# Kernel optimization log

Measured on AMD Instinct MI355X. Metric: run time of the kernel, lower is better.

Reference implementation:

```python
import jax, jax.numpy as jnp
import numpy as np

B, DIM, HH, WW = 8, 512, 64, 64
HEADS, DH = 8, 64
INNER = HEADS * DH
EPS = 1e-5  # ChanLayerNorm2D eps


def _chan_norm(x, g, b):
    # channel-wise layernorm over axis 1 (biased variance, like torch.var(unbiased=False))
    m = jnp.mean(x, axis=1, keepdims=True)
    v = jnp.mean((x - m) ** 2, axis=1, keepdims=True)
    return (x - m) / jnp.sqrt(v + EPS) * g + b


def _l2norm(x):
    # F.normalize(dim=1), eps=1e-12
    n = jnp.sqrt(jnp.sum(x * x, axis=1, keepdims=True))
    return x / jnp.maximum(n, 1e-12)


def setup_inputs() -> dict:
    key = jax.random.key(0)
    ks = jax.random.split(key, 10)
    sc = 1.0 / np.sqrt(DIM)
    return {
        "context": jax.random.normal(ks[0], (B, DIM, HH, WW), jnp.float32),
        "query_source": jax.random.normal(ks[1], (B, DIM, HH, WW), jnp.float32),
        "ctx_g": jnp.ones((1, DIM, 1, 1), jnp.float32),
        "ctx_b": jnp.zeros((1, DIM, 1, 1), jnp.float32),
        "qs_g": jnp.ones((1, DIM, 1, 1), jnp.float32),
        "qs_b": jnp.zeros((1, DIM, 1, 1), jnp.float32),
        "w_q": jax.random.normal(ks[2], (INNER, DIM), jnp.float32) * sc,
        "w_kv": jax.random.normal(ks[3], (2 * INNER, DIM), jnp.float32) * sc,
        "w_out": jax.random.normal(ks[4], (DIM, INNER), jnp.float32) * (1.0 / np.sqrt(INNER)),
        "gamma": jax.random.normal(ks[5], (1,), jnp.float32) * 0.5,
    }


def reference(context, query_source, ctx_g, ctx_b, qs_g, qs_b, w_q, w_kv, w_out, gamma):
    b, c, height, width = query_source.shape
    kh = int(height ** 0.5)  # default height_top_k
    kw = int(width ** 0.5)   # default width_top_k

    ctx = _chan_norm(context, ctx_g, ctx_b)
    qs = _chan_norm(query_source, qs_g, qs_b)

    # 1x1 convs as GEMMs
    kv = jnp.einsum('oi,bihw->bohw', w_kv, ctx)
    k, v = jnp.split(kv, 2, axis=1)
    q = jnp.einsum('oi,bihw->bohw', w_q, qs)

    def fold(t):  # b (h c) H W -> (b h) c H W
        return t.reshape(b, HEADS, DH, height, width).reshape(b * HEADS, DH, height, width)

    q, k, v = fold(q), fold(k), fold(v)
    q, k = _l2norm(q), _l2norm(k)

    # dual pruning (kh < height and kw < width here)
    q_abs = jnp.abs(q)
    k_abs = jnp.abs(k)
    q_probe = jnp.sum(q_abs, axis=(2, 3))            # (bh, c)

    # height selection
    k_height = jnp.sum(k_abs, axis=3)                # (bh, c, H)
    score_r = jnp.einsum('bc,bch->bh', q_probe, k_height)
    _, idx_h = jax.lax.top_k(score_r, kh)            # (bh, kh)
    k = jnp.take_along_axis(k, idx_h[:, None, :, None], axis=2)
    v = jnp.take_along_axis(v, idx_h[:, None, :, None], axis=2)

    # width selection (scores use pre-height-gather k_abs, as in original)
    k_width = jnp.sum(k_abs, axis=2)                 # (bh, c, W)
    score_c = jnp.einsum('bc,bcw->bw', q_probe, k_width)
    _, idx_w = jax.lax.top_k(score_c, kw)            # (bh, kw)
    k = jnp.take_along_axis(k, idx_w[:, None, None, :], axis=3)
    v = jnp.take_along_axis(v, idx_w[:, None, None, :], axis=3)

    def flat(t):  # (bh) d h w -> (bh) (h w) d
        bh, d, h_, w_ = t.shape
        return t.transpose(0, 2, 3, 1).reshape(bh, h_ * w_, d)

    qf, kf, vf = flat(q), flat(k), flat(v)
    attn = jax.nn.softmax(jnp.einsum('bid,bjd->bij', qf, kf), axis=-1)
    out = jnp.einsum('bij,bjd->bid', attn, vf)       # (bh, H*W, d)

    out = out.reshape(b, HEADS, height, width, DH).transpose(0, 1, 4, 2, 3)
    out = out.reshape(b, INNER, height, width)
    out = jnp.einsum('oi,bihw->bohw', w_out, out)
    return gamma[0] * out + qs
```

## Files before the change

### kernel.cpp

```cpp
#include <hip/hip_runtime.h>
#include <math.h>

#define HW 4096
#define DIM 512

typedef __attribute__((ext_vector_type(8))) short short8;
typedef __attribute__((ext_vector_type(4))) float f32x4;

__device__ inline unsigned short f2bf(float f) {
    unsigned int u = __float_as_uint(f);
    u += 0x7fff + ((u >> 16) & 1);
    return (unsigned short)(u >> 16);
}
__device__ inline float bf2f(unsigned short h) {
    return __uint_as_float(((unsigned int)h) << 16);
}
__device__ inline unsigned pack2(float a, float b) {
    return (unsigned)f2bf(a) | ((unsigned)f2bf(b) << 16);
}

__device__ inline void gld16(const void* g, void* lds) {
    __builtin_amdgcn_global_load_lds(
        (const __attribute__((address_space(1))) unsigned int*)g,
        (__attribute__((address_space(3))) unsigned int*)lds, 16, 0, 0);
}

__global__ void prep_weights(const float* __restrict__ w_q, const float* __restrict__ w_kv,
                             const float* __restrict__ w_out,
                             const float* __restrict__ ctx_g, const float* __restrict__ ctx_b,
                             const float* __restrict__ qs_g, const float* __restrict__ qs_b,
                             unsigned short* __restrict__ wq_b, unsigned short* __restrict__ wk_b,
                             unsigned short* __restrict__ wo_b, float* __restrict__ wv_g,
                             float* __restrict__ Avec, float* __restrict__ Cvec)
{
    int blk = blockIdx.x;
    int widx = blk >> 9;
    int o = blk & 511;
    int tid = threadIdx.x;
    const float *src, *g = nullptr, *beta = nullptr;
    if (widx == 0)      { src = w_q  + (size_t)o * DIM; g = qs_g;  beta = qs_b; }
    else if (widx == 1) { src = w_kv + (size_t)o * DIM; g = ctx_g; beta = ctx_b; }
    else if (widx == 2) { src = w_kv + (size_t)(512 + o) * DIM; g = ctx_g; beta = ctx_b; }
    else                { src = w_out + (size_t)o * DIM; }
    float a = 0.f, c = 0.f;
    for (int i = tid; i < DIM; i += 256) {
        float w = src[i];
        if (widx == 3) { wo_b[(size_t)o * DIM + i] = f2bf(w); continue; }
        float wg = w * g[i];
        if (widx == 0)      wq_b[(size_t)o * DIM + i] = f2bf(wg);
        else if (widx == 1) wk_b[(size_t)o * DIM + i] = f2bf(wg);
        else                wv_g[(size_t)o * DIM + i] = wg;
        a += wg; c += w * beta[i];
    }
    if (widx == 3) return;
    __shared__ float sa[256], sc[256];
    sa[tid] = a; sc[tid] = c;
    __syncthreads();
    for (int s = 128; s > 0; s >>= 1) {
        if (tid < s) { sa[tid] += sa[tid + s]; sc[tid] += sc[tid + s]; }
        __syncthreads();
    }
    if (tid == 0) { Avec[widx * 512 + o] = sa[0]; Cvec[widx * 512 + o] = sc[0]; }
}

__global__ __launch_bounds__(256) void conv_stats(
    const float* __restrict__ ctx, const float* __restrict__ qs,
    unsigned short* __restrict__ ctx_t, unsigned short* __restrict__ qs_t,
    float* __restrict__ ctx_m, float* __restrict__ ctx_r,
    float* __restrict__ qs_m, float* __restrict__ qs_r)
{
    int which = blockIdx.z;
    int b = blockIdx.y;
    int p0 = blockIdx.x * 32;
    const float* X = (which ? qs : ctx) + (size_t)b * DIM * HW;
    unsigned short* Xt = (which ? qs_t : ctx_t) + (size_t)b * HW * DIM;
    int tid = threadIdx.x;
    int pg = tid & 7;
    int cR = tid >> 3;

    const float* src0 = X + p0 + pg * 4;

    float4 s4 = {0.f, 0.f, 0.f, 0.f};
    float4 q4 = {0.f, 0.f, 0.f, 0.f};
    float4 buf[2][8];

#pragma unroll
    for (int it = 0; it < 2; it++)
#pragma unroll
        for (int j = 0; j < 8; j++)
            buf[it][j] = *(const float4*)(src0 + (size_t)(it * 256 + cR * 8 + j) * HW);

#pragma unroll
    for (int it = 0; it < 2; it++) {
        unsigned short* dst = Xt + (size_t)(p0 + pg * 4) * 512 + it * 256 + cR * 8;
        uint4 o;
        o.x = pack2(buf[it][0].x, buf[it][1].x);
        o.y = pack2(buf[it][2].x, buf[it][3].x);
        o.z = pack2(buf[it][4].x, buf[it][5].x);
        o.w = pack2(buf[it][6].x, buf[it][7].x);
        *(uint4*)(dst) = o;
        o.x = pack2(buf[it][0].y, buf[it][1].y);
        o.y = pack2(buf[it][2].y, buf[it][3].y);
        o.z = pack2(buf[it][4].y, buf[it][5].y);
        o.w = pack2(buf[it][6].y, buf[it][7].y);
        *(uint4*)(dst + 512) = o;
        o.x = pack2(buf[it][0].z, buf[it][1].z);
        o.y = pack2(buf[it][2].z, buf[it][3].z);
        o.z = pack2(buf[it][4].z, buf[it][5].z);
        o.w = pack2(buf[it][6].z, buf[it][7].z);
        *(uint4*)(dst + 1024) = o;
        o.x = pack2(buf[it][0].w, buf[it][1].w);
        o.y = pack2(buf[it][2].w, buf[it][3].w);
        o.z = pack2(buf[it][4].w, buf[it][5].w);
        o.w = pack2(buf[it][6].w, buf[it][7].w);
        *(uint4*)(dst + 1536) = o;
#pragma unroll
        for (int j = 0; j < 8; j++) {
            float4 v = buf[it][j];
            s4.x += v.x; s4.y += v.y; s4.z += v.z; s4.w += v.w;
            q4.x = fmaf(v.x, v.x, q4.x);
            q4.y = fmaf(v.y, v.y, q4.y);
            q4.z = fmaf(v.z, v.z, q4.z);
            q4.w = fmaf(v.w, v.w, q4.w);
        }
    }

#pragma unroll
    for (int off = 8; off <= 32; off <<= 1) {
        s4.x += __shfl_xor(s4.x, off, 64);
        s4.y += __shfl_xor(s4.y, off, 64);
        s4.z += __shfl_xor(s4.z, off, 64);
        s4.w += __shfl_xor(s4.w, off, 64);
        q4.x += __shfl_xor(q4.x, off, 64);
        q4.y += __shfl_xor(q4.y, off, 64);
        q4.z += __shfl_xor(q4.z, off, 64);
        q4.w += __shfl_xor(q4.w, off, 64);
    }

    __shared__ float sRed[4 * 32], qRed[4 * 32];
    int wave = tid >> 6, lane = tid & 63;
    if (lane < 8) {
        int base = wave * 32 + lane * 4;
        sRed[base + 0] = s4.x; sRed[base + 1] = s4.y;
        sRed[base + 2] = s4.z; sRed[base + 3] = s4.w;
        qRed[base + 0] = q4.x; qRed[base + 1] = q4.y;
        qRed[base + 2] = q4.z; qRed[base + 3] = q4.w;
    }
    __syncthreads();
    if (tid < 32) {
        float s = sRed[tid] + sRed[32 + tid] + sRed[64 + tid] + sRed[96 + tid];
        float q = qRed[tid] + qRed[32 + tid] + qRed[64 + tid] + qRed[96 + tid];
        float m = s * (1.0f / DIM);
        float var = q * (1.0f / DIM) - m * m;
        float r = 1.0f / sqrtf(var + 1e-5f);
        int pix = b * HW + p0 + tid;
        if (which == 0) { ctx_m[pix] = m; ctx_r[pix] = r; }
        else            { qs_m[pix]  = m; qs_r[pix]  = r; }
    }
}

template<int MODE>
__global__ __launch_bounds__(256) void gemm_mfma(
    const unsigned short* __restrict__ Wb, const unsigned short* __restrict__ Xt,
    float* __restrict__ Y, unsigned short* __restrict__ Ybf,
    const float* __restrict__ mean, const float* __restrict__ rstd,
    const float* __restrict__ Arow, const float* __restrict__ Crow,
    float* __restrict__ probe,
    const float* __restrict__ qsrc, const float* __restrict__ g,
    const float* __restrict__ beta, const float* __restrict__ gammaPtr)
{
    int b = blockIdx.z;
    int n0 = blockIdx.x * 128;
    int m0 = blockIdx.y * 128;
    const unsigned short* Xb = Xt + (size_t)b * HW * DIM;
    __shared__ uint4 AsBuf[512];
    __shared__ uint4 BsBuf[512];
    unsigned short* As = (unsigned short*)AsBuf;
    unsigned short* Bs = (unsigned short*)BsBuf;
    int tid = threadIdx.x;
    int lane = tid & 63;
    int wave = tid >> 6;
    int wbase = tid & 192;
    int wm = (wave >> 1) * 64;
    int wn = (wave & 1) * 64;
    int quad = lane >> 4;
    int l16 = lane & 15;

    int r0 = tid >> 2, c0 = (tid & 3) * 8;
    const unsigned short* pA0 = Wb + (size_t)(m0 + r0) * DIM + c0;
    const unsigned short* pA1 = Wb + (size_t)(m0 + 64 + r0) * DIM + c0;
    const unsigned short* pB0 = Xb + (size_t)(n0 + r0) * DIM + c0;
    const unsigned short* pB1 = Xb + (size_t)(n0 + 64 + r0) * DIM + c0;

    f32x4 acc[4][4];
#pragma unroll
    for (int i = 0; i < 4; i++)
#pragma unroll
        for (int j = 0; j < 4; j++) acc[i][j] = (f32x4){0.f, 0.f, 0.f, 0.f};

    for (int kt = 0; kt < 16; kt++) {
        gld16(pA0, AsBuf + wbase);
        gld16(pA1, AsBuf + 256 + wbase);
        gld16(pB0, BsBuf + wbase);
        gld16(pB1, BsBuf + 256 + wbase);
        pA0 += 32; pA1 += 32; pB0 += 32; pB1 += 32;
        __syncthreads();
        short8 af[4], bfr[4];
#pragma unroll
        for (int i = 0; i < 4; i++)
            af[i] = *(const short8*)(As + (wm + i * 16 + l16) * 32 + quad * 8);
#pragma unroll
        for (int j = 0; j < 4; j++)
            bfr[j] = *(const short8*)(Bs + (wn + j * 16 + l16) * 32 + quad * 8);
#pragma unroll
        for (int i = 0; i < 4; i++)
#pragma unroll
            for (int j = 0; j < 4; j++)
                acc[i][j] = __builtin_amdgcn_mfma_f32_16x16x32_bf16(af[i], bfr[j], acc[i][j], 0, 0, 0);
        __syncthreads();
    }

    if (MODE < 2) {
        float pa[4][4] = {};
#pragma unroll
        for (int j = 0; j < 4; j++) {
            int n = n0 + wn + j * 16 + l16;
            int pix = b * HW + n;
            float mn = mean[pix], rs = rstd[pix];
            float y[4][4];
            float s2 = 0.f;
#pragma unroll
            for (int i = 0; i < 4; i++) {
                int mb = m0 + wm + i * 16 + quad * 4;
#pragma unroll
                for (int r = 0; r < 4; r++) {
                    float v = rs * (acc[i][j][r] - mn * Arow[mb + r]) + Crow[mb + r];
                    y[i][r] = v;
                    s2 = fmaf(v, v, s2);
                }
            }
            s2 += __shfl_xor(s2, 16, 64);
            s2 += __shfl_xor(s2, 32, 64);
            float inv = 1.0f / fmaxf(sqrtf(s2), 1e-12f);
            unsigned short* orow = Ybf + (size_t)(b * HW + n) * 512 + m0 + wm + quad * 4;
#pragma unroll
            for (int i = 0; i < 4; i++) {
                float v0 = y[i][0] * inv, v1 = y[i][1] * inv;
                float v2 = y[i][2] * inv, v3 = y[i][3] * inv;
                uint2 pk; pk.x = pack2(v0, v1); pk.y = pack2(v2, v3);
                *(uint2*)(orow + i * 16) = pk;
                pa[i][0] += fabsf(v0); pa[i][1] += fabsf(v1);
                pa[i][2] += fabsf(v2); pa[i][3] += fabsf(v3);
            }
        }
#pragma unroll
        for (int i = 0; i < 4; i++)
#pragma unroll
            for (int r = 0; r < 4; r++) {
                float v = pa[i][r];
                v += __shfl_xor(v, 1, 64);
                v += __shfl_xor(v, 2, 64);
                v += __shfl_xor(v, 4, 64);
                v += __shfl_xor(v, 8, 64);
                pa[i][r] = v;
            }
        if (l16 == 0) {
#pragma unroll
            for (int i = 0; i < 4; i++)
#pragma unroll
                for (int r = 0; r < 4; r++) {
                    int m = m0 + wm + i * 16 + quad * 4 + r;
                    if (MODE == 0) atomicAdd(&probe[b * 512 + m], pa[i][r]);
                    else atomicAdd(&probe[(size_t)(b * 512 + m) * 64 + ((n0 + wn) >> 6)], pa[i][r]);
                }
        }
    } else {
        float* Yb = Y + (size_t)b * DIM * HW;
        float gamma = gammaPtr[0];
        const float* qb = qsrc + (size_t)b * DIM * HW;
#pragma unroll
        for (int j = 0; j < 4; j++) {
            int n = n0 + wn + j * 16 + l16;
            int pix = b * HW + n;
            float mn = mean[pix], rs = rstd[pix];
#pragma unroll
            for (int i = 0; i < 4; i++) {
                int mb = m0 + wm + i * 16 + quad * 4;
#pragma unroll
                for (int r = 0; r < 4; r++) {
                    int m = mb + r;
                    float qn = (qb[(size_t)m * HW + n] - mn) * rs * g[m] + beta[m];
                    Yb[(size_t)m * HW + n] = gamma * acc[i][j][r] + qn;
                }
            }
        }
    }
}

__global__ __launch_bounds__(256) void kws_kernel(const unsigned short* __restrict__ kbf,
                                                  float* __restrict__ kws)
{
    int blk = blockIdx.x;
    int b = blk >> 6, w = blk & 63;
    int tid = threadIdx.x;
    int c8 = tid & 63;
    int hq = tid >> 6;
    float a[8] = {};
    for (int hh = 0; hh < 16; hh++) {
        const unsigned short* row = kbf + ((size_t)(b * HW + (hq * 16 + hh) * 64 + w)) * 512 + c8 * 8;
        uint4 pk = *(const uint4*)row;
        const unsigned short* u = (const unsigned short*)&pk;
#pragma unroll
        for (int j = 0; j < 8; j++) a[j] += fabsf(bf2f(u[j]));
    }
    __shared__ float red[512 * 4];
#pragma unroll
    for (int j = 0; j < 8; j++) red[(c8 * 8 + j) * 4 + hq] = a[j];
    __syncthreads();
    if (tid < 256) {
        int c = tid;
        float v0 = red[c * 4] + red[c * 4 + 1] + red[c * 4 + 2] + red[c * 4 + 3];
        int c2 = tid + 256;
        float v1 = red[c2 * 4] + red[c2 * 4 + 1] + red[c2 * 4 + 2] + red[c2 * 4 + 3];
        kws[(size_t)(b * 512 + c) * 64 + w] = v0;
        kws[(size_t)(b * 512 + c2) * 64 + w] = v1;
    }
}

__global__ void score_topk(const float* __restrict__ qp, const float* __restrict__ khs,
                           const float* __restrict__ kws, int* __restrict__ idx_h, int* __restrict__ idx_w)
{
    int bh = blockIdx.x;
    int lane = threadIdx.x;
    float sr = 0.f, sc = 0.f;
    for (int c = 0; c < 64; c++) {
        float q = qp[bh * 64 + c];
        sr = fmaf(q, khs[(size_t)(bh * 64 + c) * 64 + lane], sr);
        sc = fmaf(q, kws[(size_t)(bh * 64 + c) * 64 + lane], sc);
    }
    float v = sr;
    for (int it = 0; it < 8; it++) {
        float bv = v; int bi = lane;
        for (int off = 1; off < 64; off <<= 1) {
            float ov = __shfl_xor(bv, off, 64);
            int oi = __shfl_xor(bi, off, 64);
            if (ov > bv || (ov == bv && oi < bi)) { bv = ov; bi = oi; }
        }
        if (lane == 0) idx_h[bh * 8 + it] = bi;
        if (lane == bi) v = -INFINITY;
    }
    v = sc;
    for (int it = 0; it < 8; it++) {
        float bv = v; int bi = lane;
        for (int off = 1; off < 64; off <<= 1) {
            float ov = __shfl_xor(bv, off, 64);
            int oi = __shfl_xor(bi, off, 64);
            if (ov > bv || (ov == bv && oi < bi)) { bv = ov; bi = oi; }
        }
        if (lane == 0) idx_w[bh * 8 + it] = bi;
        if (lane == bi) v = -INFINITY;
    }
}

__global__ void gather_kv(const unsigned short* __restrict__ kbf, const unsigned short* __restrict__ ctx_t,
                          const float* __restrict__ wv_g, const float* __restrict__ Av, const float* __restrict__ Cv,
                          const float* __restrict__ ctx_m, const float* __restrict__ ctx_r,
                          const int* __restrict__ idx_h, const int* __restrict__ idx_w,
                          unsigned short* __restrict__ kg, unsigned short* __restrict__ vgt)
{
    int blk = blockIdx.x;
    int bh = blk >> 6, j = blk & 63;
    int h = idx_h[bh * 8 + (j >> 3)];
    int w = idx_w[bh * 8 + (j & 7)];
    int p = h * 64 + w;
    int b = bh >> 3, head = bh & 7;
    int d = threadIdx.x;
    kg[(size_t)blk * 64 + d] = kbf[(size_t)(b * HW + p) * 512 + head * 64 + d];
    __shared__ float cx[DIM];
    const unsigned short* crow = ctx_t + (size_t)(b * HW + p) * 512;
    short8 cv = ((const short8*)crow)[d];
#pragma unroll
    for (int u = 0; u < 8; u++) cx[d * 8 + u] = bf2f((unsigned short)cv[u]);
    __syncthreads();
    int o = head * 64 + d;
    const float* wrow = wv_g + (size_t)o * DIM;
    float acc = 0.f;
    for (int i = 0; i < DIM; i++) acc = fmaf(wrow[i], cx[i], acc);
    int pix = b * HW + p;
    float v = ctx_r[pix] * (acc - ctx_m[pix] * Av[o]) + Cv[o];
    vgt[((size_t)bh * 64 + d) * 64 + j] = f2bf(v);
}

#define PROW 72
__global__ __launch_bounds__(256) void attn_mfma(
    const unsigned short* __restrict__ qbf, const unsigned short* __restrict__ kg,
    const unsigned short* __restrict__ vgt, unsigned short* __restrict__ abuf)
{
    int bh = blockIdx.y;
    int b = bh >> 3, head = bh & 7;
    int tid = threadIdx.x;
    int lane = tid & 63, wave = tid >> 6;
    int g = lane >> 4, l16 = lane & 15;
    int p0 = blockIdx.x * 256 + wave * 64;

    __shared__ unsigned short Plds[4][64 * PROW];
    unsigned short* P = Plds[wave];

    const unsigned short* kgb = kg + (size_t)bh * 4096;
    const unsigned short* vtb = vgt + (size_t)bh * 4096;
    const unsigned short* qb = qbf + (size_t)(b * HW) * 512 + head * 64;

    short8 Qf[4][2];
#pragma unroll
    for (int j = 0; j < 4; j++)
#pragma unroll
        for (int t = 0; t < 2; t++)
            Qf[j][t] = *(const short8*)(qb + (size_t)(p0 + j * 16 + l16) * 512 + t * 32 + g * 8);

    f32x4 S[4][4];
#pragma unroll
    for (int i = 0; i < 4; i++)
#pragma unroll
        for (int j = 0; j < 4; j++) S[i][j] = (f32x4){0.f, 0.f, 0.f, 0.f};
#pragma unroll
    for (int t = 0; t < 2; t++) {
        short8 Kf[4];
#pragma unroll
        for (int i = 0; i < 4; i++)
            Kf[i] = *(const short8*)(kgb + (i * 16 + l16) * 64 + t * 32 + g * 8);
#pragma unroll
        for (int i = 0; i < 4; i++)
#pragma unroll
            for (int j = 0; j < 4; j++)
                S[i][j] = __builtin_amdgcn_mfma_f32_16x16x32_bf16(Kf[i], Qf[j][t], S[i][j], 0, 0, 0);
    }

    float inv[4];
#pragma unroll
    for (int j = 0; j < 4; j++) {
        float e[4][4];
        float s = 0.f;
#pragma unroll
        for (int i = 0; i < 4; i++)
#pragma unroll
            for (int r = 0; r < 4; r++) { e[i][r] = __expf(S[i][j][r]); s += e[i][r]; }
        s += __shfl_xor(s, 16, 64);
        s += __shfl_xor(s, 32, 64);
        inv[j] = 1.0f / s;
        int row = j * 16 + l16;
#pragma unroll
        for (int i = 0; i < 4; i++) {
            uint2 pk;
            pk.x = pack2(e[i][0], e[i][1]);
            pk.y = pack2(e[i][2], e[i][3]);
            *(uint2*)(P + row * PROW + i * 16 + g * 4) = pk;
        }
    }

    f32x4 O[4][4];
#pragma unroll
    for (int i = 0; i < 4; i++)
#pragma unroll
        for (int j = 0; j < 4; j++) O[i][j] = (f32x4){0.f, 0.f, 0.f, 0.f};
#pragma unroll
    for (int t = 0; t < 2; t++) {
        short8 Vf[4], Pf[4];
#pragma unroll
        for (int i = 0; i < 4; i++)
            Vf[i] = *(const short8*)(vtb + (i * 16 + l16) * 64 + t * 32 + g * 8);
#pragma unroll
        for (int j = 0; j < 4; j++)
            Pf[j] = *(const short8*)(P + (j * 16 + l16) * PROW + t * 32 + g * 8);
#pragma unroll
        for (int i = 0; i < 4; i++)
#pragma unroll
            for (int j = 0; j < 4; j++)
                O[i][j] = __builtin_amdgcn_mfma_f32_16x16x32_bf16(Vf[i], Pf[j], O[i][j], 0, 0, 0);
    }

    unsigned short* ob = abuf + (size_t)(b * HW) * 512 + head * 64;
#pragma unroll
    for (int j = 0; j < 4; j++) {
        int p = p0 + j * 16 + l16;
#pragma unroll
        for (int i = 0; i < 4; i++) {
            uint2 pk;
            pk.x = pack2(O[i][j][0] * inv[j], O[i][j][1] * inv[j]);
            pk.y = pack2(O[i][j][2] * inv[j], O[i][j][3] * inv[j]);
            *(uint2*)(ob + (size_t)p * 512 + i * 16 + g * 4) = pk;
        }
    }
}

extern "C" void kernel_launch(void* const* d_in, const int* in_sizes, int n_in,
                              void* d_out, int out_size, void* d_ws, size_t ws_size,
                              hipStream_t stream)
{
    (void)in_sizes; (void)n_in; (void)out_size; (void)ws_size;
    const float* ctx   = (const float*)d_in[0];
    const float* qs    = (const float*)d_in[1];
    const float* ctx_g = (const float*)d_in[2];
    const float* ctx_b = (const float*)d_in[3];
    const float* qs_g  = (const float*)d_in[4];
    const float* qs_b  = (const float*)d_in[5];
    const float* w_q   = (const float*)d_in[6];
    const float* w_kv  = (const float*)d_in[7];
    const float* w_out = (const float*)d_in[8];
    const float* gamma = (const float*)d_in[9];
    float* out = (float*)d_out;

    char* base = (char*)d_ws;
    unsigned short* ctx_t = (unsigned short*)base;
    unsigned short* abuf  = ctx_t;
    unsigned short* qs_t  = (unsigned short*)(base + ((size_t)32 << 20));
    unsigned short* kbf   = qs_t;
    unsigned short* qbf   = (unsigned short*)(base + ((size_t)64 << 20));
    char* tail = base + ((size_t)96 << 20);
    unsigned short* wq_b = (unsigned short*)tail;
    unsigned short* wk_b = wq_b + 262144;
    unsigned short* wo_b = wk_b + 262144;
    float* wv_g  = (float*)(wo_b + 262144);
    float* Avec  = wv_g + 262144;
    float* Cvec  = Avec + 1536;
    float* ctx_m = Cvec + 1536;
    float* ctx_r = ctx_m + 32768;
    float* qs_m  = ctx_r + 32768;
    float* qs_r  = qs_m + 32768;
    float* qp    = qs_r + 32768;
    float* khs   = qp + 4096;
    float* kws   = khs + 262144;
    int*   idxh  = (int*)(kws + 262144);
    int*   idxw  = idxh + 512;
    unsigned short* kg  = (unsigned short*)(idxw + 512);
    unsigned short* vgt = kg + 262144;

    hipMemsetAsync(qp, 0, 4096 * sizeof(float), stream);
    hipMemsetAsync(khs, 0, 262144 * sizeof(float), stream);

    prep_weights<<<2048, 256, 0, stream>>>(w_q, w_kv, w_out, ctx_g, ctx_b, qs_g, qs_b,
                                           wq_b, wk_b, wo_b, wv_g, Avec, Cvec);
    conv_stats<<<dim3(128, 8, 2), 256, 0, stream>>>(ctx, qs, ctx_t, qs_t,
                                                    ctx_m, ctx_r, qs_m, qs_r);
    gemm_mfma<0><<<dim3(32, 4, 8), 256, 0, stream>>>(wq_b, qs_t, nullptr, qbf, qs_m, qs_r,
                                                     Avec, Cvec, qp, nullptr, nullptr, nullptr, nullptr);
    gemm_mfma<1><<<dim3(32, 4, 8), 256, 0, stream>>>(wk_b, ctx_t, nullptr, kbf, ctx_m, ctx_r,
                                                     Avec + 512, Cvec + 512, khs, nullptr, nullptr, nullptr, nullptr);
    kws_kernel<<<512, 256, 0, stream>>>(kbf, kws);
    score_topk<<<64, 64, 0, stream>>>(qp, khs, kws, idxh, idxw);
    gather_kv<<<4096, 64, 0, stream>>>(kbf, ctx_t, wv_g, Avec + 1024, Cvec + 1024,
                                       ctx_m, ctx_r, idxh, idxw, kg, vgt);
    attn_mfma<<<dim3(16, 64), 256, 0, stream>>>(qbf, kg, vgt, abuf);
    gemm_mfma<2><<<dim3(32, 4, 8), 256, 0, stream>>>(wo_b, abuf, out, nullptr, qs_m, qs_r,
                                                     nullptr, nullptr, nullptr, qs, qs_g, qs_b, gamma);
}
```

Baseline: 448.1 us.

## Merge prep kernels with memset zeroing and batch Q/K projection GEMMs into one launch

Folds weight preparation, channel-stat conversion and zeroing of the probe/height-score accumulators into a single multi-role kernel, replacing two memsets and two launches. When the workspace is large enough, K output gets its own buffer so the Q and K projection GEMMs run as one launch with 2x the blocks, which improves occupancy and removes a serial dependency. This costs extra workspace and branching inside the kernel, and falls back to two launches otherwise.

```diff
diff --git a/kernel.cpp b/kernel.cpp
--- a/kernel.cpp
+++ b/kernel.cpp
@@ -25,56 +25,69 @@
         (__attribute__((address_space(3))) unsigned int*)lds, 16, 0, 0);
 }
 
-__global__ void prep_weights(const float* __restrict__ w_q, const float* __restrict__ w_kv,
-                             const float* __restrict__ w_out,
-                             const float* __restrict__ ctx_g, const float* __restrict__ ctx_b,
-                             const float* __restrict__ qs_g, const float* __restrict__ qs_b,
-                             unsigned short* __restrict__ wq_b, unsigned short* __restrict__ wk_b,
-                             unsigned short* __restrict__ wo_b, float* __restrict__ wv_g,
-                             float* __restrict__ Avec, float* __restrict__ Cvec)
-{
-    int blk = blockIdx.x;
-    int widx = blk >> 9;
-    int o = blk & 511;
-    int tid = threadIdx.x;
-    const float *src, *g = nullptr, *beta = nullptr;
-    if (widx == 0)      { src = w_q  + (size_t)o * DIM; g = qs_g;  beta = qs_b; }
-    else if (widx == 1) { src = w_kv + (size_t)o * DIM; g = ctx_g; beta = ctx_b; }
-    else if (widx == 2) { src = w_kv + (size_t)(512 + o) * DIM; g = ctx_g; beta = ctx_b; }
-    else                { src = w_out + (size_t)o * DIM; }
-    float a = 0.f, c = 0.f;
-    for (int i = tid; i < DIM; i += 256) {
-        float w = src[i];
-        if (widx == 3) { wo_b[(size_t)o * DIM + i] = f2bf(w); continue; }
-        float wg = w * g[i];
-        if (widx == 0)      wq_b[(size_t)o * DIM + i] = f2bf(wg);
-        else if (widx == 1) wk_b[(size_t)o * DIM + i] = f2bf(wg);
-        else                wv_g[(size_t)o * DIM + i] = wg;
-        a += wg; c += w * beta[i];
-    }
-    if (widx == 3) return;
-    __shared__ float sa[256], sc[256];
-    sa[tid] = a; sc[tid] = c;
-    __syncthreads();
-    for (int s = 128; s > 0; s >>= 1) {
-        if (tid < s) { sa[tid] += sa[tid + s]; sc[tid] += sc[tid + s]; }
-        __syncthreads();
-    }
-    if (tid == 0) { Avec[widx * 512 + o] = sa[0]; Cvec[widx * 512 + o] = sc[0]; }
-}
-
-__global__ __launch_bounds__(256) void conv_stats(
+__global__ __launch_bounds__(256) void prep_conv(
     const float* __restrict__ ctx, const float* __restrict__ qs,
     unsigned short* __restrict__ ctx_t, unsigned short* __restrict__ qs_t,
     float* __restrict__ ctx_m, float* __restrict__ ctx_r,
-    float* __restrict__ qs_m, float* __restrict__ qs_r)
-{
-    int which = blockIdx.z;
-    int b = blockIdx.y;
-    int p0 = blockIdx.x * 32;
+    float* __restrict__ qs_m, float* __restrict__ qs_r,
+    const float* __restrict__ w_q, const float* __restrict__ w_kv,
+    const float* __restrict__ w_out,
+    const float* __restrict__ ctx_g, const float* __restrict__ ctx_b,
+    const float* __restrict__ qs_g, const float* __restrict__ qs_b,
+    unsigned short* __restrict__ wq_b, unsigned short* __restrict__ wk_b,
+    unsigned short* __restrict__ wo_b, float* __restrict__ wv_g,
+    float* __restrict__ Avec, float* __restrict__ Cvec,
+    float* __restrict__ zbase)
+{
+    int id = blockIdx.x;
+    int tid = threadIdx.x;
+
+    __shared__ float sa[256], sc[256];
+    __shared__ float sRed[4 * 32], qRed[4 * 32];
+
+    if (id >= 4096) {
+        float4* p = (float4*)(zbase + (size_t)(id - 4096) * 4096 + tid * 16);
+        float4 z = {0.f, 0.f, 0.f, 0.f};
+        p[0] = z; p[1] = z; p[2] = z; p[3] = z;
+        return;
+    }
+
+    if (id >= 2048) {
+        int blk = id - 2048;
+        int widx = blk >> 9;
+        int o = blk & 511;
+        const float *src, *g = nullptr, *beta = nullptr;
+        if (widx == 0)      { src = w_q  + (size_t)o * DIM; g = qs_g;  beta = qs_b; }
+        else if (widx == 1) { src = w_kv + (size_t)o * DIM; g = ctx_g; beta = ctx_b; }
+        else if (widx == 2) { src = w_kv + (size_t)(512 + o) * DIM; g = ctx_g; beta = ctx_b; }
+        else                { src = w_out + (size_t)o * DIM; }
+        float a = 0.f, c = 0.f;
+        for (int i = tid; i < DIM; i += 256) {
+            float w = src[i];
+            if (widx == 3) { wo_b[(size_t)o * DIM + i] = f2bf(w); continue; }
+            float wg = w * g[i];
+            if (widx == 0)      wq_b[(size_t)o * DIM + i] = f2bf(wg);
+            else if (widx == 1) wk_b[(size_t)o * DIM + i] = f2bf(wg);
+            else                wv_g[(size_t)o * DIM + i] = wg;
+            a += wg; c += w * beta[i];
+        }
+        if (widx == 3) return;
+        sa[tid] = a; sc[tid] = c;
+        __syncthreads();
+        for (int s = 128; s > 0; s >>= 1) {
+            if (tid < s) { sa[tid] += sa[tid + s]; sc[tid] += sc[tid + s]; }
+            __syncthreads();
+        }
+        if (tid == 0) { Avec[widx * 512 + o] = sa[0]; Cvec[widx * 512 + o] = sc[0]; }
+        return;
+    }
+
+    int xb = id & 127;
+    int b = (id >> 7) & 7;
+    int which = id >> 10;
+    int p0 = xb * 32;
     const float* X = (which ? qs : ctx) + (size_t)b * DIM * HW;
     unsigned short* Xt = (which ? qs_t : ctx_t) + (size_t)b * HW * DIM;
-    int tid = threadIdx.x;
     int pg = tid & 7;
     int cR = tid >> 3;
 
@@ -137,7 +150,6 @@
         q4.w += __shfl_xor(q4.w, off, 64);
     }
 
-    __shared__ float sRed[4 * 32], qRed[4 * 32];
     int wave = tid >> 6, lane = tid & 63;
     if (lane < 8) {
         int base = wave * 32 + lane * 4;
@@ -159,13 +171,134 @@
     }
 }
 
-template<int MODE>
-__global__ __launch_bounds__(256) void gemm_mfma(
+__global__ __launch_bounds__(256) void gemm_proj(
+    const unsigned short* __restrict__ wq_b, const unsigned short* __restrict__ wk_b,
+    const unsigned short* __restrict__ qs_t, const unsigned short* __restrict__ ctx_t,
+    unsigned short* __restrict__ qbf, unsigned short* __restrict__ kbf,
+    const float* __restrict__ qs_m, const float* __restrict__ qs_r,
+    const float* __restrict__ ctx_m, const float* __restrict__ ctx_r,
+    const float* __restrict__ Avec, const float* __restrict__ Cvec,
+    float* __restrict__ qp, float* __restrict__ khs, int zofs)
+{
+    int z = blockIdx.z + zofs;
+    int which = z >> 3;
+    int b = z & 7;
+    const unsigned short* Wb = which ? wk_b : wq_b;
+    const unsigned short* Xb = (which ? ctx_t : qs_t) + (size_t)b * HW * DIM;
+    unsigned short* Ybf = which ? kbf : qbf;
+    const float* mean = which ? ctx_m : qs_m;
+    const float* rstd = which ? ctx_r : qs_r;
+    const float* Arow = Avec + (which << 9);
+    const float* Crow = Cvec + (which << 9);
+
+    int n0 = blockIdx.x * 128;
+    int m0 = blockIdx.y * 128;
+    __shared__ uint4 AsBuf[512];
+    __shared__ uint4 BsBuf[512];
+    unsigned short* As = (unsigned short*)AsBuf;
+    unsigned short* Bs = (unsigned short*)BsBuf;
+    int tid = threadIdx.x;
+    int lane = tid & 63;
+    int wave = tid >> 6;
+    int wbase = tid & 192;
+    int wm = (wave >> 1) * 64;
+    int wn = (wave & 1) * 64;
+    int quad = lane >> 4;
+    int l16 = lane & 15;
+
+    int r0 = tid >> 2, c0 = (tid & 3) * 8;
+    const unsigned short* pA0 = Wb + (size_t)(m0 + r0) * DIM + c0;
+    const unsigned short* pA1 = Wb + (size_t)(m0 + 64 + r0) * DIM + c0;
+    const unsigned short* pB0 = Xb + (size_t)(n0 + r0) * DIM + c0;
+    const unsigned short* pB1 = Xb + (size_t)(n0 + 64 + r0) * DIM + c0;
+
+    f32x4 acc[4][4];
+#pragma unroll
+    for (int i = 0; i < 4; i++)
+#pragma unroll
+        for (int j = 0; j < 4; j++) acc[i][j] = (f32x4){0.f, 0.f, 0.f, 0.f};
+
+    for (int kt = 0; kt < 16; kt++) {
+        gld16(pA0, AsBuf + wbase);
+        gld16(pA1, AsBuf + 256 + wbase);
+        gld16(pB0, BsBuf + wbase);
+        gld16(pB1, BsBuf + 256 + wbase);
+        pA0 += 32; pA1 += 32; pB0 += 32; pB1 += 32;
+        __syncthreads();
+        short8 af[4], bfr[4];
+#pragma unroll
+        for (int i = 0; i < 4; i++)
+            af[i] = *(const short8*)(As + (wm + i * 16 + l16) * 32 + quad * 8);
+#pragma unroll
+        for (int j = 0; j < 4; j++)
+            bfr[j] = *(const short8*)(Bs + (wn + j * 16 + l16) * 32 + quad * 8);
+#pragma unroll
+        for (int i = 0; i < 4; i++)
+#pragma unroll
+            for (int j = 0; j < 4; j++)
+                acc[i][j] = __builtin_amdgcn_mfma_f32_16x16x32_bf16(af[i], bfr[j], acc[i][j], 0, 0, 0);
+        __syncthreads();
+    }
+
+    float pa[4][4] = {};
+#pragma unroll
+    for (int j = 0; j < 4; j++) {
+        int n = n0 + wn + j * 16 + l16;
+        int pix = b * HW + n;
+        float mn = mean[pix], rs = rstd[pix];
+        float y[4][4];
+        float s2 = 0.f;
+#pragma unroll
+        for (int i = 0; i < 4; i++) {
+            int mb = m0 + wm + i * 16 + quad * 4;
+#pragma unroll
+            for (int r = 0; r < 4; r++) {
+                float v = rs * (acc[i][j][r] - mn * Arow[mb + r]) + Crow[mb + r];
+                y[i][r] = v;
+                s2 = fmaf(v, v, s2);
+            }
+        }
+        s2 += __shfl_xor(s2, 16, 64);
+        s2 += __shfl_xor(s2, 32, 64);
+        float inv = 1.0f / fmaxf(sqrtf(s2), 1e-12f);
+        unsigned short* orow = Ybf + (size_t)(b * HW + n) * 512 + m0 + wm + quad * 4;
+#pragma unroll
+        for (int i = 0; i < 4; i++) {
+            float v0 = y[i][0] * inv, v1 = y[i][1] * inv;
+            float v2 = y[i][2] * inv, v3 = y[i][3] * inv;
+            uint2 pk; pk.x = pack2(v0, v1); pk.y = pack2(v2, v3);
+            *(uint2*)(orow + i * 16) = pk;
+            pa[i][0] += fabsf(v0); pa[i][1] += fabsf(v1);
+            pa[i][2] += fabsf(v2); pa[i][3] += fabsf(v3);
+        }
+    }
+#pragma unroll
+    for (int i = 0; i < 4; i++)
+#pragma unroll
+        for (int r = 0; r < 4; r++) {
+            float v = pa[i][r];
+            v += __shfl_xor(v, 1, 64);
+            v += __shfl_xor(v, 2, 64);
+            v += __shfl_xor(v, 4, 64);
+            v += __shfl_xor(v, 8, 64);
+            pa[i][r] = v;
+        }
+    if (l16 == 0) {
+#pragma unroll
+        for (int i = 0; i < 4; i++)
+#pragma unroll
+            for (int r = 0; r < 4; r++) {
+                int m = m0 + wm + i * 16 + quad * 4 + r;
+                if (which == 0) atomicAdd(&qp[b * 512 + m], pa[i][r]);
+                else atomicAdd(&khs[(size_t)(b * 512 + m) * 64 + ((n0 + wn) >> 6)], pa[i][r]);
+            }
+    }
+}
+
+__global__ __launch_bounds__(256) void gemm_out(
     const unsigned short* __restrict__ Wb, const unsigned short* __restrict__ Xt,
-    float* __restrict__ Y, unsigned short* __restrict__ Ybf,
+    float* __restrict__ Y,
     const float* __restrict__ mean, const float* __restrict__ rstd,
-    const float* __restrict__ Arow, const float* __restrict__ Crow,
-    float* __restrict__ probe,
     const float* __restrict__ qsrc, const float* __restrict__ g,
     const float* __restrict__ beta, const float* __restrict__ gammaPtr)
 {
@@ -220,78 +353,22 @@
         __syncthreads();
     }
 
-    if (MODE < 2) {
-        float pa[4][4] = {};
-#pragma unroll
-        for (int j = 0; j < 4; j++) {
-            int n = n0 + wn + j * 16 + l16;
-            int pix = b * HW + n;
-            float mn = mean[pix], rs = rstd[pix];
-            float y[4][4];
-            float s2 = 0.f;
-#pragma unroll
-            for (int i = 0; i < 4; i++) {
-                int mb = m0 + wm + i * 16 + quad * 4;
-#pragma unroll
-                for (int r = 0; r < 4; r++) {
-                    float v = rs * (acc[i][j][r] - mn * Arow[mb + r]) + Crow[mb + r];
-                    y[i][r] = v;
-                    s2 = fmaf(v, v, s2);
-                }
-            }
-            s2 += __shfl_xor(s2, 16, 64);
-            s2 += __shfl_xor(s2, 32, 64);
-            float inv = 1.0f / fmaxf(sqrtf(s2), 1e-12f);
-            unsigned short* orow = Ybf + (size_t)(b * HW + n) * 512 + m0 + wm + quad * 4;
-#pragma unroll
-            for (int i = 0; i < 4; i++) {
-                float v0 = y[i][0] * inv, v1 = y[i][1] * inv;
-                float v2 = y[i][2] * inv, v3 = y[i][3] * inv;
-                uint2 pk; pk.x = pack2(v0, v1); pk.y = pack2(v2, v3);
-                *(uint2*)(orow + i * 16) = pk;
-                pa[i][0] += fabsf(v0); pa[i][1] += fabsf(v1);
-                pa[i][2] += fabsf(v2); pa[i][3] += fabsf(v3);
-            }
-        }
-#pragma unroll
-        for (int i = 0; i < 4; i++)
+    float* Yb = Y + (size_t)b * DIM * HW;
+    float gamma = gammaPtr[0];
+    const float* qb = qsrc + (size_t)b * DIM * HW;
+#pragma unroll
+    for (int j = 0; j < 4; j++) {
+        int n = n0 + wn + j * 16 + l16;
+        int pix = b * HW + n;
+        float mn = mean[pix], rs = rstd[pix];
+#pragma unroll
+        for (int i = 0; i < 4; i++) {
+            int mb = m0 + wm + i * 16 + quad * 4;
 #pragma unroll
             for (int r = 0; r < 4; r++) {
-                float v = pa[i][r];
-                v += __shfl_xor(v, 1, 64);
-                v += __shfl_xor(v, 2, 64);
-                v += __shfl_xor(v, 4, 64);
-                v += __shfl_xor(v, 8, 64);
-                pa[i][r] = v;
-            }
-        if (l16 == 0) {
-#pragma unroll
-            for (int i = 0; i < 4; i++)
-#pragma unroll
-                for (int r = 0; r < 4; r++) {
-                    int m = m0 + wm + i * 16 + quad * 4 + r;
-                    if (MODE == 0) atomicAdd(&probe[b * 512 + m], pa[i][r]);
-                    else atomicAdd(&probe[(size_t)(b * 512 + m) * 64 + ((n0 + wn) >> 6)], pa[i][r]);
-                }
-        }
-    } else {
-        float* Yb = Y + (size_t)b * DIM * HW;
-        float gamma = gammaPtr[0];
-        const float* qb = qsrc + (size_t)b * DIM * HW;
-#pragma unroll
-        for (int j = 0; j < 4; j++) {
-            int n = n0 + wn + j * 16 + l16;
-            int pix = b * HW + n;
-            float mn = mean[pix], rs = rstd[pix];
-#pragma unroll
-            for (int i = 0; i < 4; i++) {
-                int mb = m0 + wm + i * 16 + quad * 4;
-#pragma unroll
-                for (int r = 0; r < 4; r++) {
-                    int m = mb + r;
-                    float qn = (qb[(size_t)m * HW + n] - mn) * rs * g[m] + beta[m];
-                    Yb[(size_t)m * HW + n] = gamma * acc[i][j][r] + qn;
-                }
+                int m = mb + r;
+                float qn = (qb[(size_t)m * HW + n] - mn) * rs * g[m] + beta[m];
+                Yb[(size_t)m * HW + n] = gamma * acc[i][j][r] + qn;
             }
         }
     }
@@ -496,7 +573,7 @@
                               void* d_out, int out_size, void* d_ws, size_t ws_size,
                               hipStream_t stream)
 {
-    (void)in_sizes; (void)n_in; (void)out_size; (void)ws_size;
+    (void)in_sizes; (void)n_in; (void)out_size;
     const float* ctx   = (const float*)d_in[0];
     const float* qs    = (const float*)d_in[1];
     const float* ctx_g = (const float*)d_in[2];
@@ -510,12 +587,15 @@
     float* out = (float*)d_out;
 
     char* base = (char*)d_ws;
+    bool sep = ws_size >= ((size_t)136 << 20);
+
     unsigned short* ctx_t = (unsigned short*)base;
     unsigned short* abuf  = ctx_t;
     unsigned short* qs_t  = (unsigned short*)(base + ((size_t)32 << 20));
-    unsigned short* kbf   = qs_t;
     unsigned short* qbf   = (unsigned short*)(base + ((size_t)64 << 20));
-    char* tail = base + ((size_t)96 << 20);
+    unsigned short* kbf   = sep ? (unsigned short*)(base + ((size_t)96 << 20))
+                                : qs_t;
+    char* tail = base + (sep ? ((size_t)128 << 20) : ((size_t)96 << 20));
     unsigned short* wq_b = (unsigned short*)tail;
     unsigned short* wk_b = wq_b + 262144;
     unsigned short* wo_b = wk_b + 262144;
@@ -534,22 +614,29 @@
     unsigned short* kg  = (unsigned short*)(idxw + 512);
     unsigned short* vgt = kg + 262144;
 
-    hipMemsetAsync(qp, 0, 4096 * sizeof(float), stream);
-    hipMemsetAsync(khs, 0, 262144 * sizeof(float), stream);
-
-    prep_weights<<<2048, 256, 0, stream>>>(w_q, w_kv, w_out, ctx_g, ctx_b, qs_g, qs_b,
-                                           wq_b, wk_b, wo_b, wv_g, Avec, Cvec);
-    conv_stats<<<dim3(128, 8, 2), 256, 0, stream>>>(ctx, qs, ctx_t, qs_t,
-                                                    ctx_m, ctx_r, qs_m, qs_r);
-    gemm_mfma<0><<<dim3(32, 4, 8), 256, 0, stream>>>(wq_b, qs_t, nullptr, qbf, qs_m, qs_r,
-                                                     Avec, Cvec, qp, nullptr, nullptr, nullptr, nullptr);
-    gemm_mfma<1><<<dim3(32, 4, 8), 256, 0, stream>>>(wk_b, ctx_t, nullptr, kbf, ctx_m, ctx_r,
-                                                     Avec + 512, Cvec + 512, khs, nullptr, nullptr, nullptr, nullptr);
+    prep_conv<<<4161, 256, 0, stream>>>(ctx, qs, ctx_t, qs_t,
+                                        ctx_m, ctx_r, qs_m, qs_r,
+                                        w_q, w_kv, w_out, ctx_g, ctx_b, qs_g, qs_b,
+                                        wq_b, wk_b, wo_b, wv_g, Avec, Cvec, qp);
+
+    if (sep) {
+        gemm_proj<<<dim3(32, 4, 16), 256, 0, stream>>>(
+            wq_b, wk_b, qs_t, ctx_t, qbf, kbf,
+            qs_m, qs_r, ctx_m, ctx_r, Avec, Cvec, qp, khs, 0);
+    } else {
+        gemm_proj<<<dim3(32, 4, 8), 256, 0, stream>>>(
+            wq_b, wk_b, qs_t, ctx_t, qbf, kbf,
+            qs_m, qs_r, ctx_m, ctx_r, Avec, Cvec, qp, khs, 0);
+        gemm_proj<<<dim3(32, 4, 8), 256, 0, stream>>>(
+            wq_b, wk_b, qs_t, ctx_t, qbf, kbf,
+            qs_m, qs_r, ctx_m, ctx_r, Avec, Cvec, qp, khs, 8);
+    }
+
     kws_kernel<<<512, 256, 0, stream>>>(kbf, kws);
     score_topk<<<64, 64, 0, stream>>>(qp, khs, kws, idxh, idxw);
     gather_kv<<<4096, 64, 0, stream>>>(kbf, ctx_t, wv_g, Avec + 1024, Cvec + 1024,
                                        ctx_m, ctx_r, idxh, idxw, kg, vgt);
     attn_mfma<<<dim3(16, 64), 256, 0, stream>>>(qbf, kg, vgt, abuf);
-    gemm_mfma<2><<<dim3(32, 4, 8), 256, 0, stream>>>(wo_b, abuf, out, nullptr, qs_m, qs_r,
-                                                     nullptr, nullptr, nullptr, qs, qs_g, qs_b, gamma);
-}
+    gemm_out<<<dim3(32, 4, 8), 256, 0, stream>>>(wo_b, abuf, out, qs_m, qs_r,
+                                                 qs, qs_g, qs_b, gamma);
+}
```

After: 438.1 us. 2.2% less time.
